# Performance work log

Hardware: AMD Instinct MI355X
Metric: run time of the kernel (lower is better)

Reference implementation:

```python
import jax, jax.numpy as jnp
import numpy as np

N_FACTORS = 4
N_ITERATIONS = 2
N_LAYERS = 2
N_USERS = 50000
N_ITEMS = 50000
EMB_DIM = 128
N_EDGES = 2_000_000
EPS = 1e-12


def setup_inputs() -> dict:
    key = jax.random.key(0)
    k1, k2, k3, k4 = jax.random.split(key, 4)
    n_nodes = N_USERS + N_ITEMS
    return {
        "user_emb": jax.random.normal(k1, (N_USERS, EMB_DIM), dtype=jnp.float32) * 0.1,
        "item_emb": jax.random.normal(k2, (N_ITEMS, EMB_DIM), dtype=jnp.float32) * 0.1,
        "all_h_list": jax.random.randint(k3, (N_EDGES,), 0, n_nodes, dtype=jnp.int32),
        "all_t_list": jax.random.randint(k4, (N_EDGES,), 0, n_nodes, dtype=jnp.int32),
    }


def _l2norm(x):
    # F.normalize(x, dim=1): x / max(||x||_2, eps)
    n = jnp.sqrt(jnp.sum(x * x, axis=1, keepdims=True))
    return x / jnp.maximum(n, EPS)


def _star_routing(user_emb, item_emb, h, t):
    n_nodes = user_emb.shape[0] + item_emb.shape[0]
    E = h.shape[0]
    ego = jnp.concatenate([user_emb, item_emb], axis=0)          # [N, D]
    A_values = jnp.ones((N_FACTORS, E), dtype=ego.dtype)
    all_embeddings = [ego]
    for _layer in range(N_LAYERS):
        ego_chunks = jnp.split(ego, N_FACTORS, axis=1)           # F x [N, D/F]
        layer_chunks = [None] * N_FACTORS
        for it in range(N_ITERATIONS):
            scores = jax.nn.softmax(A_values, axis=0)            # per-edge softmax over factors
            new_vals = []
            for i in range(N_FACTORS):
                v = scores[i]                                    # [E]
                deg = jax.ops.segment_sum(v, h, num_segments=n_nodes)  # row sums of A_i
                d_inv = 1.0 / jnp.sqrt(jnp.maximum(deg, EPS))    # D^{-1/2}
                x = ego_chunks[i] * d_inv[:, None]               # D_col @ e
                # A_i @ x : gather tails, weight by edge value, scatter-add to heads
                x = jax.ops.segment_sum(v[:, None] * x[t], h, num_segments=n_nodes)
                x = x * d_inv[:, None]                           # D_col @ (A @ (D_col @ e))
                layer_chunks[i] = x
                # routing logit update
                head = _l2norm(x[h])                             # [E, D/F]
                tail = _l2norm(ego_chunks[i][t])
                new_vals.append(jnp.sum(head * jnp.tanh(tail), axis=1))
            A_values = A_values + jnp.stack(new_vals, axis=0)
        ego = jnp.concatenate(layer_chunks, axis=1)
        all_embeddings.append(ego)
    # mean over [ego_0, ego_1, ..., ego_L]
    out = jnp.mean(jnp.stack(all_embeddings, axis=1), axis=1)    # [N, D]
    return out


def reference(user_emb, item_emb, all_h_list, all_t_list):
    all_emb = _star_routing(user_emb, item_emb, all_h_list, all_t_list)
    u_g = all_emb[:N_USERS]
    i_g = all_emb[N_USERS:]
    # with pick=False the '_t' (test) path is identical to the train path
    return u_g, i_g, u_g, i_g
```

## Files before the change

kernel.cpp:

```cpp
#include <hip/hip_runtime.h>
#include <cmath>

#define GS_LOOP(i, n) for (int i = blockIdx.x * blockDim.x + threadIdx.x; i < (n); i += gridDim.x * blockDim.x)

constexpr int NUSERS = 50000;
constexpr int NNODES = 100000;
constexpr int EMBD   = 128;
constexpr int NEDGE  = 2000000;
constexpr int NSCAN  = (NNODES + 1023) / 1024;

typedef float          v4f   __attribute__((ext_vector_type(4)));
typedef unsigned short v4u16 __attribute__((ext_vector_type(4)));

__device__ __forceinline__ float bf2f(unsigned short u) {
  union { unsigned int i; float f; } v; v.i = ((unsigned int)u) << 16; return v.f;
}
__device__ __forceinline__ unsigned short f2bf(float x) {
  union { float f; unsigned int i; } v; v.f = x;
  unsigned int r = v.i + 0x7FFFu + ((v.i >> 16) & 1u);
  return (unsigned short)(r >> 16);
}

__global__ __launch_bounds__(256) void init_k(const float4* __restrict__ ue4,
                                              const float4* __restrict__ ie4,
                                              float4* __restrict__ ego0,
                                              ushort4* __restrict__ Pb0,
                                              ushort4* __restrict__ Tnb0) {
  const int j = threadIdx.x & 31;
  const int u = blockIdx.x * 8 + (threadIdx.x >> 5);
  if (u >= NNODES) return;
  const float4 y = (u < NUSERS) ? ue4[(size_t)u * 32 + j]
                                : ie4[(size_t)(u - NUSERS) * 32 + j];
  ego0[(size_t)u * 32 + j] = y;
  Pb0[(size_t)u * 32 + j] = make_ushort4(f2bf(y.x), f2bf(y.y), f2bf(y.z), f2bf(y.w));
  float ss = y.x * y.x + y.y * y.y + y.z * y.z + y.w * y.w;
  ss += __shfl_xor(ss, 1, 64);
  ss += __shfl_xor(ss, 2, 64);
  ss += __shfl_xor(ss, 4, 64);
  const float inv = 1.f / fmaxf(sqrtf(ss), 1e-12f);
  Tnb0[(size_t)u * 32 + j] = make_ushort4(f2bf(tanhf(y.x * inv)), f2bf(tanhf(y.y * inv)),
                                          f2bf(tanhf(y.z * inv)), f2bf(tanhf(y.w * inv)));
}

__global__ void hist_k(const int* __restrict__ h, int* __restrict__ counts) {
  GS_LOOP(e, NEDGE) atomicAdd(&counts[h[e]], 1);
}

__global__ __launch_bounds__(1024) void scan1_k(const int* __restrict__ counts,
                                                int* __restrict__ part,
                                                int* __restrict__ bsum) {
  __shared__ int wsum[16];
  const int tid = threadIdx.x, lane = tid & 63, wid = tid >> 6;
  const int i = blockIdx.x * 1024 + tid;
  int v = (i < NNODES) ? counts[i] : 0;
  #pragma unroll
  for (int off = 1; off < 64; off <<= 1) {
    int y = __shfl_up(v, off, 64);
    if (lane >= off) v += y;
  }
  if (lane == 63) wsum[wid] = v;
  __syncthreads();
  if (wid == 0) {
    int w = (lane < 16) ? wsum[lane] : 0;
    #pragma unroll
    for (int off = 1; off < 16; off <<= 1) {
      int y = __shfl_up(w, off, 64);
      if (lane >= off) w += y;
    }
    if (lane < 16) wsum[lane] = w;
  }
  __syncthreads();
  const int incl = v + (wid ? wsum[wid - 1] : 0);
  if (i < NNODES) part[i] = incl;
  if (tid == 1023) bsum[blockIdx.x] = incl;
}

__global__ __launch_bounds__(128) void scan2_k(const int* __restrict__ bsum,
                                               int* __restrict__ boff) {
  __shared__ int s0[128], s1[128];
  const int tid = threadIdx.x;
  s0[tid] = (tid < NSCAN) ? bsum[tid] : 0;
  __syncthreads();
  int* a = s0; int* b = s1;
  for (int off = 1; off < 128; off <<= 1) {
    const int val = a[tid] + ((tid >= off) ? a[tid - off] : 0);
    b[tid] = val;
    __syncthreads();
    int* tmp = a; a = b; b = tmp;
  }
  boff[tid] = (tid == 0) ? 0 : a[tid - 1];
}

__global__ __launch_bounds__(1024) void scan3_k(const int* __restrict__ part,
                                                const int* __restrict__ boff,
                                                const int* __restrict__ counts,
                                                int* __restrict__ row_ptr,
                                                float* __restrict__ dv0) {
  const int i = blockIdx.x * 1024 + threadIdx.x;
  if (i < NNODES) {
    row_ptr[i + 1] = part[i] + boff[blockIdx.x];
    const float d = rsqrtf(fmaxf(0.25f * (float)counts[i], 1e-12f));
    v4f w = {d, d, d, d};
    *((v4f*)dv0 + i) = w;
  }
  if (i == 0) row_ptr[0] = 0;
}

__global__ void fill_k(const int* __restrict__ h, const int* __restrict__ t,
                       const int* __restrict__ row_ptr, int* __restrict__ cur,
                       int* __restrict__ csr_t) {
  GS_LOOP(e, NEDGE) {
    int u = h[e];
    int pos = row_ptr[u] + atomicAdd(&cur[u], 1);
    csr_t[pos] = t[e];
  }
}

__global__ __launch_bounds__(256) void deg_sm_k(const float* __restrict__ A,
                                                const int* __restrict__ row_ptr,
                                                unsigned short* __restrict__ c,
                                                float* __restrict__ dv) {
  const float4* A4 = (const float4*)A;
  ushort4* c4 = (ushort4*)c;
  const int g = threadIdx.x >> 4;
  const int lane16 = threadIdx.x & 15;
  const int u = blockIdx.x * 16 + g;
  if (u >= NNODES) return;
  const int beg = row_ptr[u], end = row_ptr[u + 1];
  float4 acc = make_float4(0.f, 0.f, 0.f, 0.f);
  for (int p = beg + lane16; p < end; p += 16) {
    float4 a = A4[p];
    float m = fmaxf(fmaxf(a.x, a.y), fmaxf(a.z, a.w));
    float e0 = __expf(a.x - m), e1 = __expf(a.y - m);
    float e2 = __expf(a.z - m), e3 = __expf(a.w - m);
    float inv = 1.f / (e0 + e1 + e2 + e3);
    float4 s = make_float4(e0 * inv, e1 * inv, e2 * inv, e3 * inv);
    c4[p] = make_ushort4(f2bf(s.x), f2bf(s.y), f2bf(s.z), f2bf(s.w));
    acc.x += s.x; acc.y += s.y; acc.z += s.z; acc.w += s.w;
  }
  #pragma unroll
  for (int m = 1; m < 16; m <<= 1) {
    acc.x += __shfl_xor(acc.x, m, 64);
    acc.y += __shfl_xor(acc.y, m, 64);
    acc.z += __shfl_xor(acc.z, m, 64);
    acc.w += __shfl_xor(acc.w, m, 64);
  }
  if (lane16 == 0)
    ((float4*)dv)[u] = make_float4(rsqrtf(fmaxf(acc.x, 1e-12f)),
                                   rsqrtf(fmaxf(acc.y, 1e-12f)),
                                   rsqrtf(fmaxf(acc.z, 1e-12f)),
                                   rsqrtf(fmaxf(acc.w, 1e-12f)));
}

template <int MODE, bool FIRST>
__global__ __launch_bounds__(256) void prop_k(
    const ushort4* __restrict__ Pb4, float4* __restrict__ Q4,
    const float* __restrict__ dv_in, const int* __restrict__ row_ptr,
    const int* __restrict__ csr_t, const unsigned short* __restrict__ c,
    float* __restrict__ A, const ushort4* __restrict__ Tnb4,
    const float4* __restrict__ e0_4, const float4* __restrict__ e1_4,
    float4* __restrict__ o1_4, ushort4* __restrict__ Pb1w,
    ushort4* __restrict__ Tnb1w) {
  const int u = blockIdx.x * 4 + (threadIdx.x >> 6);
  const int l = threadIdx.x & 63;
  const int half = l >> 5;
  const int j = l & 31;
  const int f = j >> 3;
  const int beg = row_ptr[u], end = row_ptr[u + 1];

  float4 acc = make_float4(0.f, 0.f, 0.f, 0.f);
  int p = beg + half;
  for (; p + 14 < end; p += 16) {
    const int t0 = csr_t[p],      t1 = csr_t[p + 2];
    const int t2 = csr_t[p + 4],  t3 = csr_t[p + 6];
    const int t4 = csr_t[p + 8],  t5 = csr_t[p + 10];
    const int t6 = csr_t[p + 12], t7 = csr_t[p + 14];
    const ushort4 y0 = Pb4[(size_t)t0 * 32 + j];
    const ushort4 y1 = Pb4[(size_t)t1 * 32 + j];
    const ushort4 y2 = Pb4[(size_t)t2 * 32 + j];
    const ushort4 y3 = Pb4[(size_t)t3 * 32 + j];
    const ushort4 y4 = Pb4[(size_t)t4 * 32 + j];
    const ushort4 y5 = Pb4[(size_t)t5 * 32 + j];
    const ushort4 y6 = Pb4[(size_t)t6 * 32 + j];
    const ushort4 y7 = Pb4[(size_t)t7 * 32 + j];
    const float c0 = (FIRST ? 0.25f : bf2f(__builtin_nontemporal_load(c + (size_t)p * 4 + f)))        * dv_in[t0 * 4 + f];
    const float c1 = (FIRST ? 0.25f : bf2f(__builtin_nontemporal_load(c + (size_t)(p + 2) * 4 + f)))  * dv_in[t1 * 4 + f];
    const float c2 = (FIRST ? 0.25f : bf2f(__builtin_nontemporal_load(c + (size_t)(p + 4) * 4 + f)))  * dv_in[t2 * 4 + f];
    const float c3 = (FIRST ? 0.25f : bf2f(__builtin_nontemporal_load(c + (size_t)(p + 6) * 4 + f)))  * dv_in[t3 * 4 + f];
    const float c4_ = (FIRST ? 0.25f : bf2f(__builtin_nontemporal_load(c + (size_t)(p + 8) * 4 + f))) * dv_in[t4 * 4 + f];
    const float c5 = (FIRST ? 0.25f : bf2f(__builtin_nontemporal_load(c + (size_t)(p + 10) * 4 + f))) * dv_in[t5 * 4 + f];
    const float c6 = (FIRST ? 0.25f : bf2f(__builtin_nontemporal_load(c + (size_t)(p + 12) * 4 + f))) * dv_in[t6 * 4 + f];
    const float c7 = (FIRST ? 0.25f : bf2f(__builtin_nontemporal_load(c + (size_t)(p + 14) * 4 + f))) * dv_in[t7 * 4 + f];
    acc.x += c0 * bf2f(y0.x) + c1 * bf2f(y1.x) + c2 * bf2f(y2.x) + c3 * bf2f(y3.x)
           + c4_ * bf2f(y4.x) + c5 * bf2f(y5.x) + c6 * bf2f(y6.x) + c7 * bf2f(y7.x);
    acc.y += c0 * bf2f(y0.y) + c1 * bf2f(y1.y) + c2 * bf2f(y2.y) + c3 * bf2f(y3.y)
           + c4_ * bf2f(y4.y) + c5 * bf2f(y5.y) + c6 * bf2f(y6.y) + c7 * bf2f(y7.y);
    acc.z += c0 * bf2f(y0.z) + c1 * bf2f(y1.z) + c2 * bf2f(y2.z) + c3 * bf2f(y3.z)
           + c4_ * bf2f(y4.z) + c5 * bf2f(y5.z) + c6 * bf2f(y6.z) + c7 * bf2f(y7.z);
    acc.w += c0 * bf2f(y0.w) + c1 * bf2f(y1.w) + c2 * bf2f(y2.w) + c3 * bf2f(y3.w)
           + c4_ * bf2f(y4.w) + c5 * bf2f(y5.w) + c6 * bf2f(y6.w) + c7 * bf2f(y7.w);
  }
  for (; p < end; p += 2) {
    const int tn = csr_t[p];
    const float cf = (FIRST ? 0.25f : bf2f(__builtin_nontemporal_load(c + (size_t)p * 4 + f))) * dv_in[tn * 4 + f];
    const ushort4 y = Pb4[(size_t)tn * 32 + j];
    acc.x += cf * bf2f(y.x); acc.y += cf * bf2f(y.y);
    acc.z += cf * bf2f(y.z); acc.w += cf * bf2f(y.w);
  }
  acc.x += __shfl_xor(acc.x, 32, 64);
  acc.y += __shfl_xor(acc.y, 32, 64);
  acc.z += __shfl_xor(acc.z, 32, 64);
  acc.w += __shfl_xor(acc.w, 32, 64);
  const float du = dv_in[u * 4 + f];
  const float4 x = make_float4(acc.x * du, acc.y * du, acc.z * du, acc.w * du);

  if (MODE == 2) {
    if (half == 0) {
      const v4f a = __builtin_nontemporal_load((const v4f*)e0_4 + (size_t)u * 32 + j);
      const v4f b = __builtin_nontemporal_load((const v4f*)e1_4 + (size_t)u * 32 + j);
      v4f r = {(a.x + b.x + x.x) * (1.f / 3.f), (a.y + b.y + x.y) * (1.f / 3.f),
               (a.z + b.z + x.z) * (1.f / 3.f), (a.w + b.w + x.w) * (1.f / 3.f)};
      __builtin_nontemporal_store(r, (v4f*)o1_4 + (size_t)u * 32 + j);
    }
    return;
  }
  if (MODE == 1 && half == 0) {
    v4f xq = {x.x, x.y, x.z, x.w};
    __builtin_nontemporal_store(xq, (v4f*)Q4 + (size_t)u * 32 + j);
    v4u16 pb = {f2bf(x.x), f2bf(x.y), f2bf(x.z), f2bf(x.w)};
    __builtin_nontemporal_store(pb, (v4u16*)Pb1w + (size_t)u * 32 + j);
  }

  float ss = x.x * x.x + x.y * x.y + x.z * x.z + x.w * x.w;
  ss += __shfl_xor(ss, 1, 64);
  ss += __shfl_xor(ss, 2, 64);
  ss += __shfl_xor(ss, 4, 64);
  const float inv = 1.f / fmaxf(sqrtf(ss), 1e-12f);
  const float4 xn = make_float4(x.x * inv, x.y * inv, x.z * inv, x.w * inv);
  if (MODE == 1 && half == 0) {
    v4u16 tb = {f2bf(tanhf(xn.x)), f2bf(tanhf(xn.y)), f2bf(tanhf(xn.z)), f2bf(tanhf(xn.w))};
    __builtin_nontemporal_store(tb, (v4u16*)Tnb1w + (size_t)u * 32 + j);
  }

  int q = beg + half;
  for (; q + 6 < end; q += 8) {
    const int t0 = csr_t[q],     t1 = csr_t[q + 2];
    const int t2 = csr_t[q + 4], t3 = csr_t[q + 6];
    const ushort4 b0 = Tnb4[(size_t)t0 * 32 + j];
    const ushort4 b1 = Tnb4[(size_t)t1 * 32 + j];
    const ushort4 b2 = Tnb4[(size_t)t2 * 32 + j];
    const ushort4 b3 = Tnb4[(size_t)t3 * 32 + j];
    float s0 = xn.x * bf2f(b0.x) + xn.y * bf2f(b0.y) + xn.z * bf2f(b0.z) + xn.w * bf2f(b0.w);
    float s1 = xn.x * bf2f(b1.x) + xn.y * bf2f(b1.y) + xn.z * bf2f(b1.z) + xn.w * bf2f(b1.w);
    float s2 = xn.x * bf2f(b2.x) + xn.y * bf2f(b2.y) + xn.z * bf2f(b2.z) + xn.w * bf2f(b2.w);
    float s3 = xn.x * bf2f(b3.x) + xn.y * bf2f(b3.y) + xn.z * bf2f(b3.z) + xn.w * bf2f(b3.w);
    #pragma unroll
    for (int m = 1; m < 8; m <<= 1) {
      s0 += __shfl_xor(s0, m, 64); s1 += __shfl_xor(s1, m, 64);
      s2 += __shfl_xor(s2, m, 64); s3 += __shfl_xor(s3, m, 64);
    }
    if ((j & 7) == 0) {
      if (FIRST) {
        A[(size_t)q * 4 + f] = 1.f + s0;
        A[(size_t)(q + 2) * 4 + f] = 1.f + s1;
        A[(size_t)(q + 4) * 4 + f] = 1.f + s2;
        A[(size_t)(q + 6) * 4 + f] = 1.f + s3;
      } else {
        A[(size_t)q * 4 + f] += s0;
        A[(size_t)(q + 2) * 4 + f] += s1;
        A[(size_t)(q + 4) * 4 + f] += s2;
        A[(size_t)(q + 6) * 4 + f] += s3;
      }
    }
  }
  for (; q < end; q += 2) {
    const int tn = csr_t[q];
    const ushort4 tb = Tnb4[(size_t)tn * 32 + j];
    float s = xn.x * bf2f(tb.x) + xn.y * bf2f(tb.y) + xn.z * bf2f(tb.z) + xn.w * bf2f(tb.w);
    s += __shfl_xor(s, 1, 64);
    s += __shfl_xor(s, 2, 64);
    s += __shfl_xor(s, 4, 64);
    if ((j & 7) == 0) {
      if (FIRST) A[(size_t)q * 4 + f] = 1.f + s;
      else       A[(size_t)q * 4 + f] += s;
    }
  }
}

extern "C" void kernel_launch(void* const* d_in, const int* in_sizes, int n_in,
                              void* d_out, int out_size, void* d_ws, size_t ws_size,
                              hipStream_t stream) {
  const float* ue = (const float*)d_in[0];
  const float* ie = (const float*)d_in[1];
  const int* h = (const int*)d_in[2];
  const int* t = (const int*)d_in[3];
  float* out = (float*)d_out;
  char* ws = (char*)d_ws;

  size_t off = 0;
  auto alloc = [&](size_t bytes) -> void* {
    void* p = ws + off;
    off += (bytes + 255) & ~size_t(255);
    return p;
  };
  float* ego0  = (float*)alloc(sizeof(float) * (size_t)NNODES * EMBD);
  float* ego1  = (float*)alloc(sizeof(float) * (size_t)NNODES * EMBD);
  float* A     = (float*)alloc(sizeof(float) * 4 * (size_t)NEDGE);
  unsigned short* c = (unsigned short*)alloc(sizeof(unsigned short) * 4 * (size_t)NEDGE);
  float* dvA   = (float*)alloc(sizeof(float) * NNODES * 4);
  float* dvB   = (float*)alloc(sizeof(float) * NNODES * 4);
  int* row_ptr = (int*)alloc(sizeof(int) * (NNODES + 1));
  int* cur     = (int*)alloc(sizeof(int) * NNODES);
  int* part    = (int*)alloc(sizeof(int) * NNODES);
  int* bsum    = (int*)alloc(sizeof(int) * 128);
  int* boff    = (int*)alloc(sizeof(int) * 128);
  int* csr_t   = (int*)alloc(sizeof(int) * NEDGE);

  float* o1 = out;
  float* o2 = out + (size_t)NNODES * EMBD;
  ushort4* Pb0  = (ushort4*)o1;
  ushort4* Tnb0 = (ushort4*)((char*)o1 + sizeof(unsigned short) * (size_t)NNODES * EMBD);
  ushort4* Pb1  = (ushort4*)o2;
  ushort4* Tnb1 = (ushort4*)((char*)o2 + sizeof(unsigned short) * (size_t)NNODES * EMBD);

  init_k<<<(NNODES + 7) / 8, 256, 0, stream>>>((const float4*)ue, (const float4*)ie,
                                               (float4*)ego0, Pb0, Tnb0);
  hipMemsetAsync(cur, 0, sizeof(int) * NNODES, stream);
  hist_k<<<2048, 256, 0, stream>>>(h, cur);
  scan1_k<<<NSCAN, 1024, 0, stream>>>(cur, part, bsum);
  scan2_k<<<1, 128, 0, stream>>>(bsum, boff);
  scan3_k<<<NSCAN, 1024, 0, stream>>>(part, boff, cur, row_ptr, dvA);
  hipMemsetAsync(cur, 0, sizeof(int) * NNODES, stream);
  fill_k<<<2048, 256, 0, stream>>>(h, t, row_ptr, cur, csr_t);

  prop_k<0, true><<<NNODES / 4, 256, 0, stream>>>(
      Pb0, (float4*)ego1, dvA, row_ptr, csr_t, c, A, Tnb0,
      (const float4*)ego0, (const float4*)ego1, (float4*)o1, Pb1, Tnb1);

  deg_sm_k<<<(NNODES + 15) / 16, 256, 0, stream>>>(A, row_ptr, c, dvB);
  prop_k<1, false><<<NNODES / 4, 256, 0, stream>>>(
      Pb0, (float4*)ego1, dvB, row_ptr, csr_t, c, A, Tnb0,
      (const float4*)ego0, (const float4*)ego1, (float4*)o1, Pb1, Tnb1);

  deg_sm_k<<<(NNODES + 15) / 16, 256, 0, stream>>>(A, row_ptr, c, dvA);
  prop_k<0, false><<<NNODES / 4, 256, 0, stream>>>(
      Pb1, (float4*)ego1, dvA, row_ptr, csr_t, c, A, Tnb1,
      (const float4*)ego0, (const float4*)ego1, (float4*)o1, Pb1, Tnb1);

  deg_sm_k<<<(NNODES + 15) / 16, 256, 0, stream>>>(A, row_ptr, c, dvB);
  prop_k<2, false><<<NNODES / 4, 256, 0, stream>>>(
      Pb1, (float4*)ego1, dvB, row_ptr, csr_t, c, A, Tnb1,
      (const float4*)ego0, (const float4*)ego1, (float4*)o1, Pb1, Tnb1);

  hipMemcpyAsync(o2, o1, sizeof(float) * (size_t)NNODES * EMBD,
                 hipMemcpyDeviceToDevice, stream);
}
```

Measured before the change: 1.191 ms.

## Recompute tanh of normalized tails from cached bf16 rows in LDS stash

Drops the precomputed bf16 tanh(normalized tail) table. Instead it stores a per-node, per-factor inverse-norm scale and recomputes tanh on the fly with exp2 and a reciprocal. The tail rows gathered during propagation are stashed in shared memory, up to 32 edges per node, and reused in the routing-score pass. This cuts a second random gather of tail rows and the table writes. In exchange it adds transcendental math per element, 32KB of LDS per block that may lower occupancy, and a less unrolled score loop.

```diff
diff --git a/kernel.cpp b/kernel.cpp
--- a/kernel.cpp
+++ b/kernel.cpp
@@ -8,6 +8,7 @@
 constexpr int EMBD   = 128;
 constexpr int NEDGE  = 2000000;
 constexpr int NSCAN  = (NNODES + 1023) / 1024;
+constexpr int ECAP   = 32;
 
 typedef float          v4f   __attribute__((ext_vector_type(4)));
 typedef unsigned short v4u16 __attribute__((ext_vector_type(4)));
@@ -20,12 +21,17 @@
   unsigned int r = v.i + 0x7FFFu + ((v.i >> 16) & 1u);
   return (unsigned short)(r >> 16);
 }
+__device__ __forceinline__ float tnh(unsigned short u, float nvs) {
+  const float E = exp2f(bf2f(u) * nvs);
+  return 1.f - 2.f * __builtin_amdgcn_rcpf(E + 1.f);
+}
+constexpr float TSCL = 2.f * 1.44269504088896f;
 
 __global__ __launch_bounds__(256) void init_k(const float4* __restrict__ ue4,
                                               const float4* __restrict__ ie4,
                                               float4* __restrict__ ego0,
                                               ushort4* __restrict__ Pb0,
-                                              ushort4* __restrict__ Tnb0) {
+                                              float* __restrict__ nv0) {
   const int j = threadIdx.x & 31;
   const int u = blockIdx.x * 8 + (threadIdx.x >> 5);
   if (u >= NNODES) return;
@@ -38,8 +44,7 @@
   ss += __shfl_xor(ss, 2, 64);
   ss += __shfl_xor(ss, 4, 64);
   const float inv = 1.f / fmaxf(sqrtf(ss), 1e-12f);
-  Tnb0[(size_t)u * 32 + j] = make_ushort4(f2bf(tanhf(y.x * inv)), f2bf(tanhf(y.y * inv)),
-                                          f2bf(tanhf(y.z * inv)), f2bf(tanhf(y.w * inv)));
+  if ((j & 7) == 0) nv0[u * 4 + (j >> 3)] = TSCL * inv;
 }
 
 __global__ void hist_k(const int* __restrict__ h, int* __restrict__ counts) {
@@ -155,17 +160,19 @@
 template <int MODE, bool FIRST>
 __global__ __launch_bounds__(256) void prop_k(
     const ushort4* __restrict__ Pb4, float4* __restrict__ Q4,
-    const float* __restrict__ dv_in, const int* __restrict__ row_ptr,
-    const int* __restrict__ csr_t, const unsigned short* __restrict__ c,
-    float* __restrict__ A, const ushort4* __restrict__ Tnb4,
+    const float* __restrict__ dv_in, const float* __restrict__ nv_in,
+    const int* __restrict__ row_ptr, const int* __restrict__ csr_t,
+    const unsigned short* __restrict__ c, float* __restrict__ A,
     const float4* __restrict__ e0_4, const float4* __restrict__ e1_4,
     float4* __restrict__ o1_4, ushort4* __restrict__ Pb1w,
-    ushort4* __restrict__ Tnb1w) {
+    float* __restrict__ nv1w) {
+  __shared__ ushort4 stash[4 * ECAP * 32];
   const int u = blockIdx.x * 4 + (threadIdx.x >> 6);
   const int l = threadIdx.x & 63;
   const int half = l >> 5;
   const int j = l & 31;
   const int f = j >> 3;
+  const int wbase = (threadIdx.x >> 6) * (ECAP * 32);
   const int beg = row_ptr[u], end = row_ptr[u + 1];
 
   float4 acc = make_float4(0.f, 0.f, 0.f, 0.f);
@@ -183,6 +190,17 @@
     const ushort4 y5 = Pb4[(size_t)t5 * 32 + j];
     const ushort4 y6 = Pb4[(size_t)t6 * 32 + j];
     const ushort4 y7 = Pb4[(size_t)t7 * 32 + j];
+    if (MODE != 2) {
+      const int sl = p - beg;
+      if (sl      < ECAP) stash[wbase + (sl     ) * 32 + j] = y0;
+      if (sl + 2  < ECAP) stash[wbase + (sl + 2 ) * 32 + j] = y1;
+      if (sl + 4  < ECAP) stash[wbase + (sl + 4 ) * 32 + j] = y2;
+      if (sl + 6  < ECAP) stash[wbase + (sl + 6 ) * 32 + j] = y3;
+      if (sl + 8  < ECAP) stash[wbase + (sl + 8 ) * 32 + j] = y4;
+      if (sl + 10 < ECAP) stash[wbase + (sl + 10) * 32 + j] = y5;
+      if (sl + 12 < ECAP) stash[wbase + (sl + 12) * 32 + j] = y6;
+      if (sl + 14 < ECAP) stash[wbase + (sl + 14) * 32 + j] = y7;
+    }
     const float c0 = (FIRST ? 0.25f : bf2f(__builtin_nontemporal_load(c + (size_t)p * 4 + f)))        * dv_in[t0 * 4 + f];
     const float c1 = (FIRST ? 0.25f : bf2f(__builtin_nontemporal_load(c + (size_t)(p + 2) * 4 + f)))  * dv_in[t1 * 4 + f];
     const float c2 = (FIRST ? 0.25f : bf2f(__builtin_nontemporal_load(c + (size_t)(p + 4) * 4 + f)))  * dv_in[t2 * 4 + f];
@@ -204,6 +222,10 @@
     const int tn = csr_t[p];
     const float cf = (FIRST ? 0.25f : bf2f(__builtin_nontemporal_load(c + (size_t)p * 4 + f))) * dv_in[tn * 4 + f];
     const ushort4 y = Pb4[(size_t)tn * 32 + j];
+    if (MODE != 2) {
+      const int sl = p - beg;
+      if (sl < ECAP) stash[wbase + sl * 32 + j] = y;
+    }
     acc.x += cf * bf2f(y.x); acc.y += cf * bf2f(y.y);
     acc.z += cf * bf2f(y.z); acc.w += cf * bf2f(y.w);
   }
@@ -237,46 +259,40 @@
   ss += __shfl_xor(ss, 4, 64);
   const float inv = 1.f / fmaxf(sqrtf(ss), 1e-12f);
   const float4 xn = make_float4(x.x * inv, x.y * inv, x.z * inv, x.w * inv);
-  if (MODE == 1 && half == 0) {
-    v4u16 tb = {f2bf(tanhf(xn.x)), f2bf(tanhf(xn.y)), f2bf(tanhf(xn.z)), f2bf(tanhf(xn.w))};
-    __builtin_nontemporal_store(tb, (v4u16*)Tnb1w + (size_t)u * 32 + j);
-  }
+  if (MODE == 1 && half == 0 && (j & 7) == 0) nv1w[u * 4 + f] = TSCL * inv;
 
   int q = beg + half;
-  for (; q + 6 < end; q += 8) {
-    const int t0 = csr_t[q],     t1 = csr_t[q + 2];
-    const int t2 = csr_t[q + 4], t3 = csr_t[q + 6];
-    const ushort4 b0 = Tnb4[(size_t)t0 * 32 + j];
-    const ushort4 b1 = Tnb4[(size_t)t1 * 32 + j];
-    const ushort4 b2 = Tnb4[(size_t)t2 * 32 + j];
-    const ushort4 b3 = Tnb4[(size_t)t3 * 32 + j];
-    float s0 = xn.x * bf2f(b0.x) + xn.y * bf2f(b0.y) + xn.z * bf2f(b0.z) + xn.w * bf2f(b0.w);
-    float s1 = xn.x * bf2f(b1.x) + xn.y * bf2f(b1.y) + xn.z * bf2f(b1.z) + xn.w * bf2f(b1.w);
-    float s2 = xn.x * bf2f(b2.x) + xn.y * bf2f(b2.y) + xn.z * bf2f(b2.z) + xn.w * bf2f(b2.w);
-    float s3 = xn.x * bf2f(b3.x) + xn.y * bf2f(b3.y) + xn.z * bf2f(b3.z) + xn.w * bf2f(b3.w);
+  for (; q + 2 < end; q += 4) {
+    const int t0 = csr_t[q], t1 = csr_t[q + 2];
+    const int sl0 = q - beg, sl1 = sl0 + 2;
+    const ushort4 b0 = (sl0 < ECAP) ? stash[wbase + sl0 * 32 + j] : Pb4[(size_t)t0 * 32 + j];
+    const ushort4 b1 = (sl1 < ECAP) ? stash[wbase + sl1 * 32 + j] : Pb4[(size_t)t1 * 32 + j];
+    const float n0 = nv_in[t0 * 4 + f], n1 = nv_in[t1 * 4 + f];
+    float s0 = xn.x * tnh(b0.x, n0) + xn.y * tnh(b0.y, n0)
+             + xn.z * tnh(b0.z, n0) + xn.w * tnh(b0.w, n0);
+    float s1 = xn.x * tnh(b1.x, n1) + xn.y * tnh(b1.y, n1)
+             + xn.z * tnh(b1.z, n1) + xn.w * tnh(b1.w, n1);
     #pragma unroll
     for (int m = 1; m < 8; m <<= 1) {
       s0 += __shfl_xor(s0, m, 64); s1 += __shfl_xor(s1, m, 64);
-      s2 += __shfl_xor(s2, m, 64); s3 += __shfl_xor(s3, m, 64);
     }
     if ((j & 7) == 0) {
       if (FIRST) {
         A[(size_t)q * 4 + f] = 1.f + s0;
         A[(size_t)(q + 2) * 4 + f] = 1.f + s1;
-        A[(size_t)(q + 4) * 4 + f] = 1.f + s2;
-        A[(size_t)(q + 6) * 4 + f] = 1.f + s3;
       } else {
         A[(size_t)q * 4 + f] += s0;
         A[(size_t)(q + 2) * 4 + f] += s1;
-        A[(size_t)(q + 4) * 4 + f] += s2;
-        A[(size_t)(q + 6) * 4 + f] += s3;
       }
     }
   }
   for (; q < end; q += 2) {
     const int tn = csr_t[q];
-    const ushort4 tb = Tnb4[(size_t)tn * 32 + j];
-    float s = xn.x * bf2f(tb.x) + xn.y * bf2f(tb.y) + xn.z * bf2f(tb.z) + xn.w * bf2f(tb.w);
+    const int sl = q - beg;
+    const ushort4 tb = (sl < ECAP) ? stash[wbase + sl * 32 + j] : Pb4[(size_t)tn * 32 + j];
+    const float nn = nv_in[tn * 4 + f];
+    float s = xn.x * tnh(tb.x, nn) + xn.y * tnh(tb.y, nn)
+            + xn.z * tnh(tb.z, nn) + xn.w * tnh(tb.w, nn);
     s += __shfl_xor(s, 1, 64);
     s += __shfl_xor(s, 2, 64);
     s += __shfl_xor(s, 4, 64);
@@ -318,13 +334,13 @@
 
   float* o1 = out;
   float* o2 = out + (size_t)NNODES * EMBD;
-  ushort4* Pb0  = (ushort4*)o1;
-  ushort4* Tnb0 = (ushort4*)((char*)o1 + sizeof(unsigned short) * (size_t)NNODES * EMBD);
-  ushort4* Pb1  = (ushort4*)o2;
-  ushort4* Tnb1 = (ushort4*)((char*)o2 + sizeof(unsigned short) * (size_t)NNODES * EMBD);
+  ushort4* Pb0 = (ushort4*)o1;
+  float*   nv0 = (float*)((char*)o1 + sizeof(unsigned short) * (size_t)NNODES * EMBD);
+  ushort4* Pb1 = (ushort4*)o2;
+  float*   nv1 = (float*)((char*)o2 + sizeof(unsigned short) * (size_t)NNODES * EMBD);
 
   init_k<<<(NNODES + 7) / 8, 256, 0, stream>>>((const float4*)ue, (const float4*)ie,
-                                               (float4*)ego0, Pb0, Tnb0);
+                                               (float4*)ego0, Pb0, nv0);
   hipMemsetAsync(cur, 0, sizeof(int) * NNODES, stream);
   hist_k<<<2048, 256, 0, stream>>>(h, cur);
   scan1_k<<<NSCAN, 1024, 0, stream>>>(cur, part, bsum);
@@ -334,23 +350,23 @@
   fill_k<<<2048, 256, 0, stream>>>(h, t, row_ptr, cur, csr_t);
 
   prop_k<0, true><<<NNODES / 4, 256, 0, stream>>>(
-      Pb0, (float4*)ego1, dvA, row_ptr, csr_t, c, A, Tnb0,
-      (const float4*)ego0, (const float4*)ego1, (float4*)o1, Pb1, Tnb1);
+      Pb0, (float4*)ego1, dvA, nv0, row_ptr, csr_t, c, A,
+      (const float4*)ego0, (const float4*)ego1, (float4*)o1, Pb1, nv1);
 
   deg_sm_k<<<(NNODES + 15) / 16, 256, 0, stream>>>(A, row_ptr, c, dvB);
   prop_k<1, false><<<NNODES / 4, 256, 0, stream>>>(
-      Pb0, (float4*)ego1, dvB, row_ptr, csr_t, c, A, Tnb0,
-      (const float4*)ego0, (const float4*)ego1, (float4*)o1, Pb1, Tnb1);
+      Pb0, (float4*)ego1, dvB, nv0, row_ptr, csr_t, c, A,
+      (const float4*)ego0, (const float4*)ego1, (float4*)o1, Pb1, nv1);
 
   deg_sm_k<<<(NNODES + 15) / 16, 256, 0, stream>>>(A, row_ptr, c, dvA);
   prop_k<0, false><<<NNODES / 4, 256, 0, stream>>>(
-      Pb1, (float4*)ego1, dvA, row_ptr, csr_t, c, A, Tnb1,
-      (const float4*)ego0, (const float4*)ego1, (float4*)o1, Pb1, Tnb1);
+      Pb1, (float4*)ego1, dvA, nv1, row_ptr, csr_t, c, A,
+      (const float4*)ego0, (const float4*)ego1, (float4*)o1, Pb1, nv1);
 
   deg_sm_k<<<(NNODES + 15) / 16, 256, 0, stream>>>(A, row_ptr, c, dvB);
   prop_k<2, false><<<NNODES / 4, 256, 0, stream>>>(
-      Pb1, (float4*)ego1, dvB, row_ptr, csr_t, c, A, Tnb1,
-      (const float4*)ego0, (const float4*)ego1, (float4*)o1, Pb1, Tnb1);
+      Pb1, (float4*)ego1, dvB, nv1, row_ptr, csr_t, c, A,
+      (const float4*)ego0, (const float4*)ego1, (float4*)o1, Pb1, nv1);
 
   hipMemcpyAsync(o2, o1, sizeof(float) * (size_t)NNODES * EMBD,
                  hipMemcpyDeviceToDevice, stream);
```

After: 1.697 ms. 42.4% more time.
